# Kernel tuning notes

Measured on AMD Instinct MI355X. Metric: run time of the kernel, lower is better.

Reference implementation:

```python
import jax, jax.numpy as jnp
import numpy as np

B, T, D, H = 4, 2048, 1024, 16
HD = D // H


def setup_inputs() -> dict:
    key = jax.random.key(0)
    ks = jax.random.split(key, 6)
    s = 0.02
    return {
        "x": jax.random.normal(ks[0], (B, T, D), dtype=jnp.float32),
        "padding_mask": jnp.zeros((B, T), dtype=bool),
        "Wq": jax.random.normal(ks[1], (D, D), dtype=jnp.float32) * s,
        "Wk": jax.random.normal(ks[2], (D, D), dtype=jnp.float32) * s,
        "Wv": jax.random.normal(ks[3], (D, D), dtype=jnp.float32) * s,
        "Wo": jax.random.normal(ks[4], (D, D), dtype=jnp.float32) * s,
        "bo": jax.random.normal(ks[5], (D,), dtype=jnp.float32) * s,
    }


def reference(x, padding_mask, Wq, Wk, Wv, Wo, bo):
    # torch nn.Linear: y = x @ W.T
    b, t, d = x.shape
    q = (x @ Wq.T).reshape(b, t, H, HD).transpose(0, 2, 1, 3)  # [B,H,T,hd]
    k = (x @ Wk.T).reshape(b, t, H, HD).transpose(0, 2, 1, 3)
    v = (x @ Wv.T).reshape(b, t, H, HD).transpose(0, 2, 1, 3)

    scores = jnp.einsum("bhid,bhjd->bhij", q, k) / jnp.sqrt(jnp.float32(HD))
    causal = jnp.tril(jnp.ones((t, t), dtype=bool))  # [T,T]
    neg_inf = jnp.float32(-jnp.inf)
    scores = jnp.where(causal[None, None, :, :], scores, neg_inf)
    scores = jnp.where(padding_mask[:, None, None, :], neg_inf, scores)

    attn = jax.nn.softmax(scores, axis=-1)
    out = jnp.einsum("bhij,bhjd->bhid", attn, v)
    out = out.transpose(0, 2, 1, 3).reshape(b, t, d)
    out = out @ Wo.T + bo
    nonpad = (~padding_mask)[:, :, None].astype(out.dtype)
    return out * nonpad
```

## Files before the change

kernel.cpp:

```cpp
#include <hip/hip_runtime.h>

#define B_ 4
#define T_ 2048
#define D_ 1024
#define H_ 16
#define BT_ (B_ * T_)
#define QSCALE (0.125f * 1.44269504088896f)

typedef unsigned short u16;
typedef unsigned long long u64;
typedef __attribute__((ext_vector_type(8))) __bf16 bf16x8;
typedef __attribute__((ext_vector_type(4))) float f32x4;

__device__ __forceinline__ u16 f2bf(float f) {
  unsigned u = __builtin_bit_cast(unsigned, f);
  u += 0x7FFFu + ((u >> 16) & 1u);
  return (u16)(u >> 16);
}

__device__ __forceinline__ void gload16(const void* g, void* l) {
  __builtin_amdgcn_global_load_lds(
      (const __attribute__((address_space(1))) void*)g,
      (__attribute__((address_space(3))) void*)l, 16, 0, 0);
}

__global__ void cvt_bf16(const float* __restrict__ in, u16* __restrict__ out, int n4) {
  int i = blockIdx.x * 256 + threadIdx.x;
  if (i >= n4) return;
  const float4 v = ((const float4*)in)[i];
  ushort4 o;
  o.x = f2bf(v.x); o.y = f2bf(v.y); o.z = f2bf(v.z); o.w = f2bf(v.w);
  ((ushort4*)out)[i] = o;
}

__global__ void cvt_wts(const float* __restrict__ Wq, const float* __restrict__ Wk,
                        const float* __restrict__ Wv, const float* __restrict__ Wo,
                        u16* __restrict__ wdst,
                        const unsigned char* __restrict__ pm, unsigned char* __restrict__ fl) {
  const int by = blockIdx.y;
  if (by < 4) {
    const float* src = (by == 0) ? Wq : (by == 1) ? Wk : (by == 2) ? Wv : Wo;
    const int i = blockIdx.x * 256 + threadIdx.x;
    const float4 v = ((const float4*)src)[i];
    ushort4 o;
    o.x = f2bf(v.x); o.y = f2bf(v.y); o.z = f2bf(v.z); o.w = f2bf(v.w);
    ((ushort4*)(wdst + (size_t)by * D_ * D_))[i] = o;
  } else if (blockIdx.x == 0 && threadIdx.x < 128) {
    const int i = threadIdx.x;
    const unsigned long long* p = (const unsigned long long*)(pm + i * 64);
    unsigned long long acc = 0;
#pragma unroll
    for (int k = 0; k < 8; ++k) acc |= p[k];
    fl[i] = acc ? 1 : 0;
  }
}

template<int MODE>
__global__ __launch_bounds__(256, 2) void gemm_bt(
    const u16* __restrict__ A, const u16* __restrict__ Bw,
    float* __restrict__ Cf, const float* __restrict__ bias,
    const unsigned char* __restrict__ rowmask,
    u16* __restrict__ Cq, u16* __restrict__ Ck, u16* __restrict__ Cvt)
{
  __shared__ __align__(16) u16 sA[128 * 64];
  __shared__ __align__(16) u16 sB[128 * 64];
  const int tid = threadIdx.x;
  const int lane = tid & 63, wave = tid >> 6;
  const int g = lane >> 4, s15 = lane & 15;
  const int bm = blockIdx.x * 128, bn = blockIdx.y * 128;
  const int wr = wave >> 1, wc = wave & 1;

  const int srow = lane >> 3;
  const int scol = ((lane & 7) ^ srow) << 3;

  f32x4 acc[4][4] = {};

  for (int kt = 0; kt < 16; ++kt) {
    __syncthreads();
    const int k0 = kt << 6;
#pragma unroll
    for (int c = 0; c < 4; ++c) {
      const int chunk = c * 4 + wave;
      gload16(A  + (size_t)(bm + chunk * 8 + srow) * 1024 + k0 + scol, (char*)sA + chunk * 1024);
      gload16(Bw + (size_t)(bn + chunk * 8 + srow) * 1024 + k0 + scol, (char*)sB + chunk * 1024);
    }
    __syncthreads();
#pragma unroll
    for (int kk = 0; kk < 2; ++kk) {
      const int cb = ((kk << 6) | (g << 4)) ^ ((s15 & 7) << 4);
      bf16x8 af[4], bf[4];
#pragma unroll
      for (int mm = 0; mm < 4; ++mm)
        af[mm] = *(const bf16x8*)((const char*)sA + (wr * 64 + mm * 16 + s15) * 128 + cb);
#pragma unroll
      for (int nn = 0; nn < 4; ++nn)
        bf[nn] = *(const bf16x8*)((const char*)sB + (wc * 64 + nn * 16 + s15) * 128 + cb);
#pragma unroll
      for (int mm = 0; mm < 4; ++mm)
#pragma unroll
        for (int nn = 0; nn < 4; ++nn)
          acc[mm][nn] = __builtin_amdgcn_mfma_f32_16x16x32_bf16(af[mm], bf[nn], acc[mm][nn], 0, 0, 0);
    }
  }

  if (MODE == 1) {
    const int region = bn >> 10;
    const float a = (region == 0) ? QSCALE : 1.f;
#pragma unroll
    for (int mm = 0; mm < 4; ++mm)
#pragma unroll
      for (int nn = 0; nn < 4; ++nn) {
        const int col = bn + wc * 64 + nn * 16 + s15;
        const int colr = col & 1023;
        const int row0 = bm + wr * 64 + mm * 16 + (g << 2);
        if (region == 2) {
          ushort4 w;
          w.x = f2bf(acc[mm][nn][0]); w.y = f2bf(acc[mm][nn][1]);
          w.z = f2bf(acc[mm][nn][2]); w.w = f2bf(acc[mm][nn][3]);
          *(ushort4*)(Cvt + (size_t)colr * BT_ + row0) = w;
        } else {
          u16* dst = region ? Ck : Cq;
#pragma unroll
          for (int r = 0; r < 4; ++r)
            dst[(size_t)(row0 + r) * 1024 + colr] = f2bf(acc[mm][nn][r] * a);
        }
      }
  } else {
#pragma unroll
    for (int mm = 0; mm < 4; ++mm)
#pragma unroll
      for (int nn = 0; nn < 4; ++nn) {
        const int col = bn + wc * 64 + nn * 16 + s15;
        const int row0 = bm + wr * 64 + mm * 16 + (g << 2);
        const float bv = bias[col];
#pragma unroll
        for (int r = 0; r < 4; ++r) {
          float v = acc[mm][nn][r] + bv;
          v = rowmask[row0 + r] ? 0.f : v;
          Cf[(size_t)(row0 + r) * 1024 + col] = v;
        }
      }
  }
}

#define QK_TILE(T, ST) do {                                                    \
  const int kvq_ = (T) << 6;                                                   \
  _Pragma("unroll")                                                            \
  for (int jf_ = 0; jf_ < 4; ++jf_) ST[jf_] = f32x4{};                         \
  if (kvq_ <= qw + 15) {                                                       \
    const u16* kbq_ = &sK[(T) & 3][0];                                         \
    _Pragma("unroll")                                                          \
    for (int ks_ = 0; ks_ < 2; ++ks_) {                                        \
      bf16x8 kf_[4];                                                           \
      _Pragma("unroll")                                                        \
      for (int jf_ = 0; jf_ < 4; ++jf_)                                        \
        kf_[jf_] = *(const bf16x8*)(kbq_ + (jf_ * 16 + s15) * 64 +             \
                                    (((ks_ * 4 + g) ^ (s15 & 7)) << 3));       \
      __builtin_amdgcn_s_setprio(1);                                           \
      _Pragma("unroll")                                                        \
      for (int jf_ = 0; jf_ < 4; ++jf_)                                        \
        ST[jf_] = __builtin_amdgcn_mfma_f32_16x16x32_bf16(kf_[jf_], qf[ks_],   \
                                                          ST[jf_], 0, 0, 0);   \
      __builtin_amdgcn_s_setprio(0);                                           \
    }                                                                          \
  }                                                                            \
} while (0)

#define ATTN_ITER(T, CUR, NXT) do {                                            \
  const int kv0_ = (T) << 6;                                                   \
  if ((T) + 3 < nt) {                                                          \
    const int s_ = ((T) + 3) & 3;                                              \
    gload16(Kb0 + (size_t)(kv0_ + 192 + srow) * D_, (char*)(&sK[s_][0]) + tid * 16); \
    gload16(Vb0 + (size_t)srow * BT_ + kv0_ + 192,  (char*)(&sV[s_][0]) + tid * 16); \
  }                                                                            \
  if ((T) + 1 < nt) QK_TILE((T) + 1, NXT);                                     \
  if (kv0_ <= qw + 15) {                                                       \
    if (kv0_ + 63 > qw) {                                                      \
      const int iq_ = qw + s15;                                                \
      _Pragma("unroll")                                                        \
      for (int jf_ = 0; jf_ < 4; ++jf_) {                                      \
        const int jb_ = kv0_ + jf_ * 16 + g * 4;                               \
        _Pragma("unroll")                                                      \
        for (int r_ = 0; r_ < 4; ++r_)                                         \
          if (jb_ + r_ > iq_) CUR[jf_][r_] = -1e30f;                           \
      }                                                                        \
    }                                                                          \
    if ((flq[(T) >> 3] >> (((T) & 7) * 8)) & 0xff) {                           \
      _Pragma("unroll")                                                        \
      for (int jf_ = 0; jf_ < 4; ++jf_) {                                      \
        const int jb_ = kv0_ + jf_ * 16 + g * 4;                               \
        uchar4 p4_ = *(const uchar4*)(pm + b * T_ + jb_);                      \
        const unsigned char* pr_ = (const unsigned char*)&p4_;                 \
        _Pragma("unroll")                                                      \
        for (int r_ = 0; r_ < 4; ++r_)                                         \
          if (pr_[r_]) CUR[jf_][r_] = -1e30f;                                  \
      }                                                                        \
    }                                                                          \
    _Pragma("unroll")                                                          \
    for (int jf_ = 0; jf_ < 4; ++jf_) {                                        \
      _Pragma("unroll")                                                        \
      for (int r_ = 0; r_ < 4; ++r_)                                           \
        CUR[jf_][r_] = __builtin_amdgcn_exp2f(CUR[jf_][r_]);                   \
      l4 += CUR[jf_];                                                          \
    }                                                                          \
    const u16* vbq_ = &sV[(T) & 3][0];                                         \
    _Pragma("unroll")                                                          \
    for (int kb_ = 0; kb_ < 2; ++kb_) {                                        \
      bf16x8 vf_[4];                                                           \
      _Pragma("unroll")                                                        \
      for (int df_ = 0; df_ < 4; ++df_)                                        \
        vf_[df_] = *(const bf16x8*)(vbq_ + (df_ * 16 + s15) * 64 +             \
                                    (((kb_ * 4 + g) ^ (s15 & 7)) << 3));       \
      unsigned w00, w01, w10, w11;                                             \
      asm("v_cvt_pk_bf16_f32 %0, %1, %2" : "=v"(w00) : "v"(CUR[2*kb_][0]),   "v"(CUR[2*kb_][1]));   \
      asm("v_cvt_pk_bf16_f32 %0, %1, %2" : "=v"(w01) : "v"(CUR[2*kb_][2]),   "v"(CUR[2*kb_][3]));   \
      asm("v_cvt_pk_bf16_f32 %0, %1, %2" : "=v"(w10) : "v"(CUR[2*kb_+1][0]), "v"(CUR[2*kb_+1][1])); \
      asm("v_cvt_pk_bf16_f32 %0, %1, %2" : "=v"(w11) : "v"(CUR[2*kb_+1][2]), "v"(CUR[2*kb_+1][3])); \
      asm("v_permlane32_swap_b32 %0, %1" : "+v"(w00), "+v"(w10));              \
      asm("v_permlane16_swap_b32 %0, %1" : "+v"(w00), "+v"(w10));              \
      asm("v_permlane32_swap_b32 %0, %1" : "+v"(w01), "+v"(w11));              \
      asm("v_permlane16_swap_b32 %0, %1" : "+v"(w01), "+v"(w11));              \
      union { unsigned u[4]; bf16x8 v; } pf_;                                  \
      pf_.u[0] = w00; pf_.u[1] = w01; pf_.u[2] = w10; pf_.u[3] = w11;          \
      __builtin_amdgcn_s_setprio(1);                                           \
      _Pragma("unroll")                                                        \
      for (int df_ = 0; df_ < 4; ++df_)                                        \
        o[df_] = __builtin_amdgcn_mfma_f32_16x16x32_bf16(vf_[df_], pf_.v,      \
                                                         o[df_], 0, 0, 0);     \
      __builtin_amdgcn_s_setprio(0);                                           \
    }                                                                          \
  }                                                                            \
  if ((T) + 1 < nt) {                                                          \
    if ((T) + 3 < nt) asm volatile("s_waitcnt vmcnt(2) lgkmcnt(0)" ::: "memory"); \
    else              asm volatile("s_waitcnt vmcnt(0) lgkmcnt(0)" ::: "memory"); \
    __builtin_amdgcn_s_barrier();                                              \
    asm volatile("" ::: "memory");                                             \
  }                                                                            \
} while (0)

__global__ __launch_bounds__(512, 4) void attn_fwd(
    const u16* __restrict__ Q, const u16* __restrict__ K,
    const u16* __restrict__ VT, const unsigned char* __restrict__ pm,
    const unsigned char* __restrict__ tileflag, u16* __restrict__ O)
{
  __shared__ __align__(16) u16 sK[4][64 * 64];
  __shared__ __align__(16) u16 sV[4][64 * 64];
  const int tid = threadIdx.x;
  const int lane = tid & 63, wave = tid >> 6;
  const int g = lane >> 4, s15 = lane & 15;
  const int bh = blockIdx.x, b = bh >> 4, h = bh & 15;
  const int jpair = blockIdx.y;
  const size_t tokbase = (size_t)b * T_;

  const int srow = tid >> 3;
  const int sc = (tid & 7) ^ (srow & 7);
  const u16* Kb0 = K + tokbase * D_ + h * 64 + sc * 8;
  const u16* Vb0 = VT + (size_t)(h * 64) * BT_ + tokbase + sc * 8;

  u64 flq[4];
#pragma unroll
  for (int q = 0; q < 4; ++q) flq[q] = ((const u64*)(tileflag + b * 32))[q];

#pragma unroll
  for (int half = 0; half < 2; ++half) {
    const int qt = half ? (15 - jpair) : jpair;
    const int qw = qt * 128 + wave * 16;
    const int nt = 2 * qt + 2;

    bf16x8 qf[2];
#pragma unroll
    for (int ks = 0; ks < 2; ++ks)
      qf[ks] = *(const bf16x8*)(Q + (tokbase + qw + s15) * D_ + h * 64 + ks * 32 + g * 8);

    f32x4 o[4] = {};
    f32x4 l4 = {};

    __syncthreads();
#pragma unroll
    for (int s = 0; s < 3; ++s) {
      gload16(Kb0 + (size_t)(s * 64 + srow) * D_, (char*)(&sK[s][0]) + tid * 16);
      gload16(Vb0 + (size_t)srow * BT_ + s * 64,  (char*)(&sV[s][0]) + tid * 16);
    }
    asm volatile("s_waitcnt vmcnt(2) lgkmcnt(0)" ::: "memory");
    __builtin_amdgcn_s_barrier();
    asm volatile("" ::: "memory");

    f32x4 stA[4], stB[4];
    QK_TILE(0, stA);

    for (int t = 0; t < nt; t += 2) {
      ATTN_ITER(t, stA, stB);
      ATTN_ITER(t + 1, stB, stA);
    }

    float lv = (l4[0] + l4[1]) + (l4[2] + l4[3]);
    lv += __shfl_xor(lv, 16);
    lv += __shfl_xor(lv, 32);
    const float inv = 1.f / lv;
    u16* orow = O + (tokbase + qw + s15) * D_ + h * 64 + g * 4;
#pragma unroll
    for (int df = 0; df < 4; ++df) {
      ushort4 w;
      w.x = f2bf(o[df][0] * inv); w.y = f2bf(o[df][1] * inv);
      w.z = f2bf(o[df][2] * inv); w.w = f2bf(o[df][3] * inv);
      *(ushort4*)(orow + df * 16) = w;
    }
  }
}

extern "C" void kernel_launch(void* const* d_in, const int* in_sizes, int n_in,
                              void* d_out, int out_size, void* d_ws, size_t ws_size,
                              hipStream_t stream)
{
  const float* x  = (const float*)d_in[0];
  const unsigned char* pm = (const unsigned char*)d_in[1];
  const float* Wq = (const float*)d_in[2];
  const float* Wk = (const float*)d_in[3];
  const float* Wv = (const float*)d_in[4];
  const float* Wo = (const float*)d_in[5];
  const float* bo = (const float*)d_in[6];
  float* out = (float*)d_out;

  char* w = (char*)d_ws;
  u16* xb  = (u16*)w; w += (size_t)BT_ * D_ * 2;
  u16* wqb = (u16*)w; w += (size_t)D_ * D_ * 2;
  u16* wkb = (u16*)w; w += (size_t)D_ * D_ * 2;
  u16* wvb = (u16*)w; w += (size_t)D_ * D_ * 2;
  u16* wob = (u16*)w; w += (size_t)D_ * D_ * 2;
  u16* qb  = (u16*)w; w += (size_t)BT_ * D_ * 2;
  u16* kbf = (u16*)w; w += (size_t)BT_ * D_ * 2;
  u16* vt  = (u16*)w; w += (size_t)BT_ * D_ * 2;
  u16* ao  = (u16*)w; w += (size_t)BT_ * D_ * 2;
  unsigned char* flags = (unsigned char*)w; w += 256;
  (void)wkb; (void)wvb;

  const int nx4 = BT_ * D_ / 4;
  cvt_bf16<<<nx4 / 256, 256, 0, stream>>>(x, xb, nx4);
  cvt_wts<<<dim3(1024, 5), 256, 0, stream>>>(Wq, Wk, Wv, Wo, wqb, pm, flags);

  gemm_bt<1><<<dim3(64, 24), 256, 0, stream>>>(xb, wqb, nullptr, nullptr, nullptr, qb, kbf, vt);

  attn_fwd<<<dim3(B_ * H_, 8), 512, 0, stream>>>(qb, kbf, vt, pm, flags, ao);

  gemm_bt<0><<<dim3(64, 8), 256, 0, stream>>>(ao, wob, out, bo, pm, nullptr, nullptr, nullptr);
}
```

Measured before the change: 142.8 us.

## Use 256x256 multi-stage pipelined QKV GEMM and merge conversion kernels

Replaces the QKV projection GEMM with a 512-thread kernel that computes a 256x256 tile, keeps a 4-slot LDS ring filled by asynchronous global-to-LDS loads, and splits each k-step into four phases so prefetch overlaps MFMA work. This targets per-tile load stalls and low data reuse in the old 128x128 kernel. The input and weight conversion kernels are also merged into one launch to save a launch. The larger tile uses 128KB of LDS and gives a grid of only 384 blocks, so occupancy and tail balance may suffer.

```diff
diff --git a/kernel.cpp b/kernel.cpp
--- a/kernel.cpp
+++ b/kernel.cpp
@@ -24,43 +24,162 @@
       (__attribute__((address_space(3))) void*)l, 16, 0, 0);
 }
 
-__global__ void cvt_bf16(const float* __restrict__ in, u16* __restrict__ out, int n4) {
-  int i = blockIdx.x * 256 + threadIdx.x;
-  if (i >= n4) return;
-  const float4 v = ((const float4*)in)[i];
-  ushort4 o;
-  o.x = f2bf(v.x); o.y = f2bf(v.y); o.z = f2bf(v.z); o.w = f2bf(v.w);
-  ((ushort4*)out)[i] = o;
-}
-
-__global__ void cvt_wts(const float* __restrict__ Wq, const float* __restrict__ Wk,
+__global__ void cvt_all(const float* __restrict__ x,
+                        const float* __restrict__ Wq, const float* __restrict__ Wk,
                         const float* __restrict__ Wv, const float* __restrict__ Wo,
-                        u16* __restrict__ wdst,
+                        u16* __restrict__ xb, u16* __restrict__ wdst,
                         const unsigned char* __restrict__ pm, unsigned char* __restrict__ fl) {
-  const int by = blockIdx.y;
-  if (by < 4) {
-    const float* src = (by == 0) ? Wq : (by == 1) ? Wk : (by == 2) ? Wv : Wo;
-    const int i = blockIdx.x * 256 + threadIdx.x;
+  const int fb = blockIdx.x;
+  if (fb < 8192) {
+    const int i = fb * 256 + threadIdx.x;
+    const float4 v = ((const float4*)x)[i];
+    ushort4 o;
+    o.x = f2bf(v.x); o.y = f2bf(v.y); o.z = f2bf(v.z); o.w = f2bf(v.w);
+    ((ushort4*)xb)[i] = o;
+  } else if (fb < 12288) {
+    const int wsel = (fb - 8192) >> 10;
+    const float* src = (wsel == 0) ? Wq : (wsel == 1) ? Wk : (wsel == 2) ? Wv : Wo;
+    const int i = ((fb - 8192) & 1023) * 256 + threadIdx.x;
     const float4 v = ((const float4*)src)[i];
     ushort4 o;
     o.x = f2bf(v.x); o.y = f2bf(v.y); o.z = f2bf(v.z); o.w = f2bf(v.w);
-    ((ushort4*)(wdst + (size_t)by * D_ * D_))[i] = o;
-  } else if (blockIdx.x == 0 && threadIdx.x < 128) {
+    ((ushort4*)(wdst + (size_t)wsel * D_ * D_))[i] = o;
+  } else if (threadIdx.x < 128) {
     const int i = threadIdx.x;
-    const unsigned long long* p = (const unsigned long long*)(pm + i * 64);
-    unsigned long long acc = 0;
+    const u64* p = (const u64*)(pm + i * 64);
+    u64 acc = 0;
 #pragma unroll
     for (int k = 0; k < 8; ++k) acc |= p[k];
     fl[i] = acc ? 1 : 0;
   }
 }
 
-template<int MODE>
-__global__ __launch_bounds__(256, 2) void gemm_bt(
+__global__ __launch_bounds__(512, 2) void gemm_qkv8(
+    const u16* __restrict__ A, const u16* __restrict__ Bw,
+    u16* __restrict__ Cq, u16* __restrict__ Ck, u16* __restrict__ Cvt)
+{
+  __shared__ __align__(16) u16 sA[4][128 * 64];
+  __shared__ __align__(16) u16 sB[4][128 * 64];
+  const int tid = threadIdx.x;
+  const int lane = tid & 63, wave = tid >> 6;
+  const int g = lane >> 4, s15 = lane & 15;
+  const int wm = wave >> 2, wn = wave & 3;
+  const int bm = blockIdx.x * 256, bn = blockIdx.y * 256;
+
+  int rowL[2], colL[2];
+#pragma unroll
+  for (int l = 0; l < 2; ++l) {
+    const int chunk = tid + l * 512;
+    rowL[l] = chunk >> 3;
+    colL[l] = ((chunk & 7) ^ (rowL[l] & 7)) << 3;
+  }
+
+#define SA_(H) do {                                                            \
+    const int k0_ = ((H) >> 1) << 6;                                           \
+    const size_t r0_ = (size_t)(bm + ((H) & 1) * 128);                         \
+    char* d_ = (char*)&sA[(H) & 3][0] + tid * 16;                              \
+    gload16(A + (r0_ + rowL[0]) * 1024 + k0_ + colL[0], d_);                   \
+    gload16(A + (r0_ + rowL[1]) * 1024 + k0_ + colL[1], d_ + 8192);            \
+  } while (0)
+#define SB_(H) do {                                                            \
+    const int k0_ = ((H) >> 1) << 6;                                           \
+    const size_t r0_ = (size_t)(bn + ((H) & 1) * 128);                         \
+    char* d_ = (char*)&sB[(H) & 3][0] + tid * 16;                              \
+    gload16(Bw + (r0_ + rowL[0]) * 1024 + k0_ + colL[0], d_);                  \
+    gload16(Bw + (r0_ + rowL[1]) * 1024 + k0_ + colL[1], d_ + 8192);           \
+  } while (0)
+
+  f32x4 acc[2][2][4][2] = {};
+
+  SA_(0); SB_(0); SA_(1); SB_(1); SA_(2); SB_(2); SA_(3); SB_(3);
+  asm volatile("s_waitcnt vmcnt(8)" ::: "memory");
+  __builtin_amdgcn_s_barrier();
+  asm volatile("" ::: "memory");
+
+  for (int t = 0; t < 16; ++t) {
+    const int H2 = 2 * t;
+
+#define PHASE(MH, NH) do {                                                     \
+      const u16* aS_ = &sA[(H2 + (MH)) & 3][0];                                \
+      const u16* bS_ = &sB[(H2 + (NH)) & 3][0];                                \
+      bf16x8 af_[4][2], bf_[2][2];                                             \
+      _Pragma("unroll")                                                        \
+      for (int kk = 0; kk < 2; ++kk) {                                         \
+        const int cb_ = ((kk * 4 + g) ^ (s15 & 7)) << 4;                       \
+        _Pragma("unroll")                                                      \
+        for (int m = 0; m < 4; ++m)                                            \
+          af_[m][kk] = *(const bf16x8*)((const char*)aS_ +                     \
+                         (wm * 64 + m * 16 + s15) * 128 + cb_);                \
+        _Pragma("unroll")                                                      \
+        for (int n = 0; n < 2; ++n)                                            \
+          bf_[n][kk] = *(const bf16x8*)((const char*)bS_ +                     \
+                         (wn * 32 + n * 16 + s15) * 128 + cb_);                \
+      }                                                                        \
+      if ((MH) == 0 && (NH) == 0) { if (t >= 1 && t <= 14) SA_(H2 + 3); }      \
+      if ((MH) == 0 && (NH) == 1) { if (t >= 1 && t <= 14) SB_(H2 + 3); }      \
+      if ((MH) == 1 && (NH) == 0) { if (t <= 13) SA_(H2 + 4); }                \
+      if ((MH) == 1 && (NH) == 1) { if (t <= 13) SB_(H2 + 4); }                \
+      __builtin_amdgcn_s_barrier();                                            \
+      asm volatile("s_waitcnt lgkmcnt(0)" ::: "memory");                       \
+      __builtin_amdgcn_sched_barrier(0);                                       \
+      __builtin_amdgcn_s_setprio(1);                                           \
+      _Pragma("unroll")                                                        \
+      for (int m = 0; m < 4; ++m)                                              \
+        _Pragma("unroll")                                                      \
+        for (int n = 0; n < 2; ++n)                                            \
+          _Pragma("unroll")                                                    \
+          for (int kk = 0; kk < 2; ++kk)                                       \
+            acc[MH][NH][m][n] = __builtin_amdgcn_mfma_f32_16x16x32_bf16(       \
+                af_[m][kk], bf_[n][kk], acc[MH][NH][m][n], 0, 0, 0);           \
+      __builtin_amdgcn_s_setprio(0);                                           \
+      if ((MH) == 1 && (NH) == 1 && t < 15) {                                  \
+        if (t <= 13) asm volatile("s_waitcnt vmcnt(4)" ::: "memory");          \
+        else         asm volatile("s_waitcnt vmcnt(0)" ::: "memory");          \
+      }                                                                        \
+      __builtin_amdgcn_s_barrier();                                            \
+      asm volatile("" ::: "memory");                                           \
+    } while (0)
+
+    PHASE(0, 0);
+    PHASE(0, 1);
+    PHASE(1, 0);
+    PHASE(1, 1);
+#undef PHASE
+  }
+
+  const int region = bn >> 10;
+  const float a = (region == 0) ? QSCALE : 1.f;
+#pragma unroll
+  for (int mh = 0; mh < 2; ++mh)
+#pragma unroll
+    for (int nh = 0; nh < 2; ++nh)
+#pragma unroll
+      for (int m = 0; m < 4; ++m)
+#pragma unroll
+        for (int n = 0; n < 2; ++n) {
+          const int col = bn + nh * 128 + wn * 32 + n * 16 + s15;
+          const int colr = col & 1023;
+          const int row0 = bm + mh * 128 + wm * 64 + m * 16 + (g << 2);
+          if (region == 2) {
+            ushort4 w;
+            w.x = f2bf(acc[mh][nh][m][n][0]); w.y = f2bf(acc[mh][nh][m][n][1]);
+            w.z = f2bf(acc[mh][nh][m][n][2]); w.w = f2bf(acc[mh][nh][m][n][3]);
+            *(ushort4*)(Cvt + (size_t)colr * BT_ + row0) = w;
+          } else {
+            u16* dst = region ? Ck : Cq;
+#pragma unroll
+            for (int r = 0; r < 4; ++r)
+              dst[(size_t)(row0 + r) * 1024 + colr] = f2bf(acc[mh][nh][m][n][r] * a);
+          }
+        }
+#undef SA_
+#undef SB_
+}
+
+__global__ __launch_bounds__(256, 2) void gemm_out(
     const u16* __restrict__ A, const u16* __restrict__ Bw,
     float* __restrict__ Cf, const float* __restrict__ bias,
-    const unsigned char* __restrict__ rowmask,
-    u16* __restrict__ Cq, u16* __restrict__ Ck, u16* __restrict__ Cvt)
+    const unsigned char* __restrict__ rowmask)
 {
   __shared__ __align__(16) u16 sA[128 * 64];
   __shared__ __align__(16) u16 sB[128 * 64];
@@ -103,44 +222,20 @@
     }
   }
 
-  if (MODE == 1) {
-    const int region = bn >> 10;
-    const float a = (region == 0) ? QSCALE : 1.f;
-#pragma unroll
-    for (int mm = 0; mm < 4; ++mm)
-#pragma unroll
-      for (int nn = 0; nn < 4; ++nn) {
-        const int col = bn + wc * 64 + nn * 16 + s15;
-        const int colr = col & 1023;
-        const int row0 = bm + wr * 64 + mm * 16 + (g << 2);
-        if (region == 2) {
-          ushort4 w;
-          w.x = f2bf(acc[mm][nn][0]); w.y = f2bf(acc[mm][nn][1]);
-          w.z = f2bf(acc[mm][nn][2]); w.w = f2bf(acc[mm][nn][3]);
-          *(ushort4*)(Cvt + (size_t)colr * BT_ + row0) = w;
-        } else {
-          u16* dst = region ? Ck : Cq;
-#pragma unroll
-          for (int r = 0; r < 4; ++r)
-            dst[(size_t)(row0 + r) * 1024 + colr] = f2bf(acc[mm][nn][r] * a);
-        }
+#pragma unroll
+  for (int mm = 0; mm < 4; ++mm)
+#pragma unroll
+    for (int nn = 0; nn < 4; ++nn) {
+      const int col = bn + wc * 64 + nn * 16 + s15;
+      const int row0 = bm + wr * 64 + mm * 16 + (g << 2);
+      const float bv = bias[col];
+#pragma unroll
+      for (int r = 0; r < 4; ++r) {
+        float v = acc[mm][nn][r] + bv;
+        v = rowmask[row0 + r] ? 0.f : v;
+        Cf[(size_t)(row0 + r) * 1024 + col] = v;
       }
-  } else {
-#pragma unroll
-    for (int mm = 0; mm < 4; ++mm)
-#pragma unroll
-      for (int nn = 0; nn < 4; ++nn) {
-        const int col = bn + wc * 64 + nn * 16 + s15;
-        const int row0 = bm + wr * 64 + mm * 16 + (g << 2);
-        const float bv = bias[col];
-#pragma unroll
-        for (int r = 0; r < 4; ++r) {
-          float v = acc[mm][nn][r] + bv;
-          v = rowmask[row0 + r] ? 0.f : v;
-          Cf[(size_t)(row0 + r) * 1024 + col] = v;
-        }
-      }
-  }
+    }
 }
 
 #define QK_TILE(T, ST) do {                                                    \
@@ -334,13 +429,11 @@
   unsigned char* flags = (unsigned char*)w; w += 256;
   (void)wkb; (void)wvb;
 
-  const int nx4 = BT_ * D_ / 4;
-  cvt_bf16<<<nx4 / 256, 256, 0, stream>>>(x, xb, nx4);
-  cvt_wts<<<dim3(1024, 5), 256, 0, stream>>>(Wq, Wk, Wv, Wo, wqb, pm, flags);
-
-  gemm_bt<1><<<dim3(64, 24), 256, 0, stream>>>(xb, wqb, nullptr, nullptr, nullptr, qb, kbf, vt);
+  cvt_all<<<12289, 256, 0, stream>>>(x, Wq, Wk, Wv, Wo, xb, wqb, pm, flags);
+
+  gemm_qkv8<<<dim3(32, 12), 512, 0, stream>>>(xb, wqb, qb, kbf, vt);
 
   attn_fwd<<<dim3(B_ * H_, 8), 512, 0, stream>>>(qb, kbf, vt, pm, flags, ao);
 
-  gemm_bt<0><<<dim3(64, 8), 256, 0, stream>>>(ao, wob, out, bo, pm, nullptr, nullptr, nullptr);
-}
+  gemm_out<<<dim3(64, 8), 256, 0, stream>>>(ao, wob, out, bo, pm);
+}
```

After: 169.7 us. +18.9%, slower.
